# Optimization experiments

Hardware: AMD Instinct MI355X
Metric: run time of the kernel (lower is better)

Reference implementation:

```python
import jax, jax.numpy as jnp
import numpy as np

B, L, D_IN = 8, 512, 1024
HEAD_SIZE = 64
NUM_LABELS = 16
INF = 1e12


def _rotary_sin_cos(seq_len, dim):
    # HF RoFormerSinusoidalPositionalEmbedding: inv_freq = 10000^(-2i/dim)
    pos = np.arange(seq_len, dtype=np.float64)[:, None]
    inv_freq = 1.0 / np.power(10000.0, 2.0 * np.arange(dim // 2) / dim)
    ang = pos * inv_freq  # [L, dim//2]
    # interleave: [s0, s0, s1, s1, ...] (matches stack([sin,sin],-1).reshape)
    sin = jnp.asarray(np.repeat(np.sin(ang), 2, axis=-1), dtype=jnp.float32)
    cos = jnp.asarray(np.repeat(np.cos(ang), 2, axis=-1), dtype=jnp.float32)
    return sin[None], cos[None]  # [1, L, dim]


def _rotate_half(x):
    # [-x1, x0, -x3, x2, ...]
    return jnp.stack([-x[..., 1::2], x[..., ::2]], axis=-1).reshape(x.shape)


def setup_inputs() -> dict:
    key = jax.random.key(0)
    k1, k2, k3, k4, k5 = jax.random.split(key, 5)
    s1 = 1.0 / np.sqrt(D_IN)
    s2 = 1.0 / np.sqrt(2 * HEAD_SIZE)
    return {
        "inputs": jax.random.normal(k1, (B, L, D_IN), dtype=jnp.float32),
        "attention_mask": jnp.ones((B, L), dtype=jnp.int32),
        "W1": jax.random.uniform(k2, (D_IN, 2 * HEAD_SIZE), jnp.float32, -s1, s1),
        "b1": jax.random.uniform(k3, (2 * HEAD_SIZE,), jnp.float32, -s1, s1),
        "W2": jax.random.uniform(k4, (2 * HEAD_SIZE, 2 * NUM_LABELS), jnp.float32, -s2, s2),
        "b2": jax.random.uniform(k5, (2 * NUM_LABELS,), jnp.float32, -s2, s2),
    }


def reference(inputs, attention_mask, W1, b1, W2, b2):
    h = inputs @ W1 + b1                      # [B, L, 2*head_size]
    qw, kw = h[..., ::2], h[..., 1::2]        # [B, L, head_size]

    sin, cos = _rotary_sin_cos(h.shape[1], HEAD_SIZE)
    qw = qw * cos + _rotate_half(qw) * sin
    kw = kw * cos + _rotate_half(kw) * sin

    logits = jnp.einsum("bmd,bnd->bmn", qw, kw) / (HEAD_SIZE ** 0.5)  # [B, L, L]

    bias = (h @ W2 + b2).transpose(0, 2, 1) / 2.0        # [B, 2*heads, L]
    logits = logits[:, None] + bias[:, ::2, None, :] + bias[:, 1::2, :, None]  # [B, heads, L, L]

    am = attention_mask.astype(logits.dtype)
    attn_mask = 1.0 - am[:, None, None, :] * am[:, None, :, None]
    logits = logits - attn_mask * INF

    tril = jnp.tril(jnp.ones((h.shape[1], h.shape[1]), logits.dtype), k=-1)
    logits = logits - tril * INF
    return logits
```

## Files before the change

### kernel.cpp

```cpp
#include <hip/hip_runtime.h>
#include <math.h>

#define B_   8
#define L_   512
#define DIN  1024
#define H_   128
#define HEAD 64
#define NL   16
#define INF_ 1.0e12f

#define SIN_OFF  0
#define COS_OFF  (512*32)
#define QROT_OFF (COS_OFF + 512*32)
#define KROT_OFF (QROT_OFF + B_*L_*HEAD)
#define BQ_OFF   (KROT_OFF + B_*L_*HEAD)
#define BK_OFF   (BQ_OFF + B_*NL*L_)
#define W1T_OFF  (BK_OFF + B_*NL*L_)
#define W2T_OFF  (W1T_OFF + 65536)

typedef float          floatx4  __attribute__((ext_vector_type(4)));
typedef short          shortx8  __attribute__((ext_vector_type(8)));
typedef unsigned short ushortx8 __attribute__((ext_vector_type(8)));

__device__ __forceinline__ unsigned short f2bf(float f) {
    unsigned u = __float_as_uint(f);
    u += 0x7FFFu + ((u >> 16) & 1u);
    return (unsigned short)(u >> 16);
}

__global__ __launch_bounds__(256) void prep_kernel(const float* __restrict__ W1,
                                                   const float* __restrict__ W2,
                                                   float* __restrict__ ws) {
    __shared__ float lds[64 * 132];
    const int tid = threadIdx.x;
    const int bid = blockIdx.x;

    if (bid < 64) {
        int idx = bid * 256 + tid;
        int m = idx >> 5, i = idx & 31;
        double ang = (double)m * pow(10000.0, -(double)i / 32.0);
        ws[SIN_OFF + idx] = (float)sin(ang);
        ws[COS_OFF + idx] = (float)cos(ang);
    } else if (bid < 80) {
        const int k0 = (bid - 64) * 64;
        for (int i = 0; i < 8; i++) {
            int f = tid + i * 256;
            int k = f >> 5, n4 = (f & 31) * 4;
            *(float4*)&lds[k * 132 + n4] = *(const float4*)&W1[(size_t)(k0 + k) * H_ + n4];
        }
        __syncthreads();
        unsigned short* W1T = (unsigned short*)(ws + W1T_OFF);
        const int n  = tid >> 1;
        const int kh = (tid & 1) * 32;
        for (int i = 0; i < 4; i++) {
            ushortx8 p;
            #pragma unroll
            for (int j = 0; j < 8; j++) p[j] = f2bf(lds[(kh + i * 8 + j) * 132 + n]);
            *(ushortx8*)&W1T[(size_t)n * DIN + k0 + kh + i * 8] = p;
        }
    } else {
        unsigned short* W2T = (unsigned short*)(ws + W2T_OFF);
        const int o  = tid >> 3;
        const int kc = (tid & 7) * 16;
        ushortx8 p0, p1;
        #pragma unroll
        for (int j = 0; j < 8; j++) p0[j] = f2bf(W2[(size_t)(kc + j) * 32 + o]);
        #pragma unroll
        for (int j = 0; j < 8; j++) p1[j] = f2bf(W2[(size_t)(kc + 8 + j) * 32 + o]);
        *(ushortx8*)&W2T[(size_t)o * H_ + kc]     = p0;
        *(ushortx8*)&W2T[(size_t)o * H_ + kc + 8] = p1;
    }
}

__global__ __launch_bounds__(256) void gemm1_fused_kernel(
    const float* __restrict__ X, const float* __restrict__ b1,
    const float* __restrict__ b2, float* __restrict__ ws)
{
    __shared__ float hs[16 * 132];

    const int tid  = threadIdx.x;
    const int m0   = blockIdx.x * 16;
    const int w    = tid >> 6;
    const int lane = tid & 63;
    const int lrow = lane >> 4;
    const int lcol = lane & 15;

    const unsigned short* W1T = (const unsigned short*)(ws + W1T_OFF);

    const float* pA = X + (size_t)(m0 + lcol) * DIN + lrow * 8;
    const unsigned short* pB0 = W1T + (size_t)(w * 32 + lcol) * DIN + lrow * 8;
    const unsigned short* pB1 = pB0 + (size_t)16 * DIN;

    floatx4 acc0 = {0.f, 0.f, 0.f, 0.f};
    floatx4 acc1 = {0.f, 0.f, 0.f, 0.f};

    #pragma unroll
    for (int s = 0; s < 32; s++) {
        float4 a0 = *(const float4*)(pA + s * 32);
        float4 a1 = *(const float4*)(pA + s * 32 + 4);
        shortx8 bf0 = *(const shortx8*)(pB0 + s * 32);
        shortx8 bf1 = *(const shortx8*)(pB1 + s * 32);
        ushortx8 afu;
        afu[0] = f2bf(a0.x); afu[1] = f2bf(a0.y); afu[2] = f2bf(a0.z); afu[3] = f2bf(a0.w);
        afu[4] = f2bf(a1.x); afu[5] = f2bf(a1.y); afu[6] = f2bf(a1.z); afu[7] = f2bf(a1.w);
        shortx8 af = (shortx8)afu;
        acc0 = __builtin_amdgcn_mfma_f32_16x16x32_bf16(af, bf0, acc0, 0, 0, 0);
        acc1 = __builtin_amdgcn_mfma_f32_16x16x32_bf16(af, bf1, acc1, 0, 0, 0);
    }

    {
        float b1a = b1[w * 32 + lcol];
        float b1b = b1[w * 32 + 16 + lcol];
        #pragma unroll
        for (int r = 0; r < 4; r++) {
            hs[(lrow * 4 + r) * 132 + w * 32 + lcol]      = acc0[r] + b1a;
            hs[(lrow * 4 + r) * 132 + w * 32 + 16 + lcol] = acc1[r] + b1b;
        }
    }
    __syncthreads();

    {
        int row = tid >> 4;
        int j   = tid & 15;
        int g   = m0 + row;
        int pos = g & (L_ - 1);
        const float* hr = &hs[row * 132];
        float h0 = hr[8 * j + 0], h1 = hr[8 * j + 1];
        float h2 = hr[8 * j + 2], h3 = hr[8 * j + 3];
        float h4 = hr[8 * j + 4], h5 = hr[8 * j + 5];
        float h6 = hr[8 * j + 6], h7 = hr[8 * j + 7];
        float s0 = ws[SIN_OFF + pos * 32 + 2 * j];
        float c0 = ws[COS_OFF + pos * 32 + 2 * j];
        float s1 = ws[SIN_OFF + pos * 32 + 2 * j + 1];
        float c1 = ws[COS_OFF + pos * 32 + 2 * j + 1];
        float4 q, k;
        q.x = h0 * c0 - h2 * s0;  q.y = h2 * c0 + h0 * s0;
        q.z = h4 * c1 - h6 * s1;  q.w = h6 * c1 + h4 * s1;
        k.x = h1 * c0 - h3 * s0;  k.y = h3 * c0 + h1 * s0;
        k.z = h5 * c1 - h7 * s1;  k.w = h7 * c1 + h5 * s1;
        *(float4*)&ws[QROT_OFF + (size_t)g * HEAD + 4 * j] = q;
        *(float4*)&ws[KROT_OFF + (size_t)g * HEAD + 4 * j] = k;
    }

    if (w == 0) {
        const unsigned short* W2T = (const unsigned short*)(ws + W2T_OFF);
        floatx4 bacc0 = {0.f, 0.f, 0.f, 0.f};
        floatx4 bacc1 = {0.f, 0.f, 0.f, 0.f};
        #pragma unroll
        for (int s = 0; s < 4; s++) {
            int k = s * 32 + lrow * 8;
            ushortx8 hfu;
            #pragma unroll
            for (int j = 0; j < 8; j++) hfu[j] = f2bf(hs[lcol * 132 + k + j]);
            shortx8 hf = (shortx8)hfu;
            shortx8 wf0 = *(const shortx8*)(W2T + (size_t)lcol * H_ + k);
            shortx8 wf1 = *(const shortx8*)(W2T + (size_t)(16 + lcol) * H_ + k);
            bacc0 = __builtin_amdgcn_mfma_f32_16x16x32_bf16(hf, wf0, bacc0, 0, 0, 0);
            bacc1 = __builtin_amdgcn_mfma_f32_16x16x32_bf16(hf, wf1, bacc1, 0, 0, 0);
        }
        float b2a = b2[lcol], b2b = b2[16 + lcol];
        #pragma unroll
        for (int r = 0; r < 4; r++) {
            int g   = m0 + lrow * 4 + r;
            int bb  = g >> 9;
            int pos = g & (L_ - 1);
            float v0 = (bacc0[r] + b2a) * 0.5f;
            float v1 = (bacc1[r] + b2b) * 0.5f;
            int o0 = lcol, o1 = 16 + lcol;
            if (o0 & 1) ws[BQ_OFF + ((size_t)bb * NL + (o0 >> 1)) * L_ + pos] = v0;
            else        ws[BK_OFF + ((size_t)bb * NL + (o0 >> 1)) * L_ + pos] = v0;
            if (o1 & 1) ws[BQ_OFF + ((size_t)bb * NL + (o1 >> 1)) * L_ + pos] = v1;
            else        ws[BK_OFF + ((size_t)bb * NL + (o1 >> 1)) * L_ + pos] = v1;
        }
    }
}

__global__ __launch_bounds__(256) void qk_bcast_kernel(
    const int* __restrict__ am, const float* __restrict__ ws, float* __restrict__ out)
{
    __shared__ float Qs[64][68];
    __shared__ float Ks[64][68];
    __shared__ float BQs[16][64];
    __shared__ float BKs[16][64];
    __shared__ float maskM[64];
    __shared__ float maskN[64];

    const int tid = threadIdx.x;
    const int bid = blockIdx.x;
    const int bb = bid >> 6;
    const int mt = (bid >> 3) & 7;
    const int nt = bid & 7;
    const int m0 = mt * 64, n0 = nt * 64;

    {
        int r0   = tid >> 4;
        int dcol = (tid & 15) * 4;
        #pragma unroll
        for (int rr = 0; rr < 4; rr++) {
            int r = r0 + rr * 16;
            float4 q = *(const float4*)&ws[QROT_OFF + ((size_t)(bb * L_ + m0 + r)) * HEAD + dcol];
            float4 k = *(const float4*)&ws[KROT_OFF + ((size_t)(bb * L_ + n0 + r)) * HEAD + dcol];
            Qs[dcol + 0][r] = q.x; Qs[dcol + 1][r] = q.y;
            Qs[dcol + 2][r] = q.z; Qs[dcol + 3][r] = q.w;
            Ks[dcol + 0][r] = k.x; Ks[dcol + 1][r] = k.y;
            Ks[dcol + 2][r] = k.z; Ks[dcol + 3][r] = k.w;
        }
    }
    {
        int l = tid >> 4;
        int c = (tid & 15) * 4;
        *(float4*)&BQs[l][c] = *(const float4*)&ws[BQ_OFF + ((size_t)bb * NL + l) * L_ + m0 + c];
        *(float4*)&BKs[l][c] = *(const float4*)&ws[BK_OFF + ((size_t)bb * NL + l) * L_ + n0 + c];
    }
    if (tid < 64)       maskM[tid]      = (float)am[bb * L_ + m0 + tid];
    else if (tid < 128) maskN[tid - 64] = (float)am[bb * L_ + n0 + (tid - 64)];
    __syncthreads();

    const int ty = tid >> 4;
    const int tx = tid & 15;
    float acc[4][4] = {};
    #pragma unroll 8
    for (int d = 0; d < HEAD; d++) {
        float4 a  = *(const float4*)&Qs[d][ty * 4];
        float4 bv = *(const float4*)&Ks[d][tx * 4];
        acc[0][0] += a.x * bv.x; acc[0][1] += a.x * bv.y; acc[0][2] += a.x * bv.z; acc[0][3] += a.x * bv.w;
        acc[1][0] += a.y * bv.x; acc[1][1] += a.y * bv.y; acc[1][2] += a.y * bv.z; acc[1][3] += a.y * bv.w;
        acc[2][0] += a.z * bv.x; acc[2][1] += a.z * bv.y; acc[2][2] += a.z * bv.z; acc[2][3] += a.z * bv.w;
        acc[3][0] += a.w * bv.x; acc[3][1] += a.w * bv.y; acc[3][2] += a.w * bv.z; acc[3][3] += a.w * bv.w;
    }

    float4 base[4];
    #pragma unroll
    for (int r = 0; r < 4; r++) {
        int m = m0 + ty * 4 + r;
        float mm = maskM[ty * 4 + r];
        #pragma unroll
        for (int c = 0; c < 4; c++) {
            int n = n0 + tx * 4 + c;
            float v = acc[r][c] * 0.125f
                    - (1.0f - mm * maskN[tx * 4 + c]) * INF_
                    - ((n < m) ? INF_ : 0.0f);
            ((float*)&base[r])[c] = v;
        }
    }

    #pragma unroll
    for (int l = 0; l < NL; l++) {
        float4 bk4 = *(const float4*)&BKs[l][tx * 4];
        size_t outb = (((size_t)(bb * NL + l)) * L_ + m0 + ty * 4) * L_ + n0 + tx * 4;
        #pragma unroll
        for (int r = 0; r < 4; r++) {
            float bq = BQs[l][ty * 4 + r];
            float4 o;
            o.x = base[r].x + bk4.x + bq;
            o.y = base[r].y + bk4.y + bq;
            o.z = base[r].z + bk4.z + bq;
            o.w = base[r].w + bk4.w + bq;
            *(float4*)&out[outb + (size_t)r * L_] = o;
        }
    }
}

extern "C" void kernel_launch(void* const* d_in, const int* in_sizes, int n_in,
                              void* d_out, int out_size, void* d_ws, size_t ws_size,
                              hipStream_t stream) {
    const float* X  = (const float*)d_in[0];
    const int*   am = (const int*)d_in[1];
    const float* W1 = (const float*)d_in[2];
    const float* b1 = (const float*)d_in[3];
    const float* W2 = (const float*)d_in[4];
    const float* b2 = (const float*)d_in[5];
    float* out = (float*)d_out;
    float* ws  = (float*)d_ws;

    prep_kernel<<<81, 256, 0, stream>>>(W1, W2, ws);
    gemm1_fused_kernel<<<(B_ * L_) / 16, 256, 0, stream>>>(X, b1, b2, ws);
    qk_bcast_kernel<<<B_ * (L_ / 64) * (L_ / 64), 256, 0, stream>>>(am, ws, out);
}
```

Before: 53.91 us.

## Split GEMM1 K dimension across 16 waves with LDS reduction; float rotary tables

The projection GEMM now runs with 1024-thread blocks. The K=1024 reduction is split four ways across wave groups, and the partial MFMA accumulators are summed in shared memory before the bias and rotary epilogue. This raises memory-level parallelism per row tile, at the cost of a 32KB LDS reduction buffer and an extra barrier. Separately, the sin/cos table generation switches from double-precision pow/sin/cos to single-precision expf/sinf/cosf to cut prep cost, with a small risk to accuracy at large angles.

```diff
diff --git a/kernel.cpp b/kernel.cpp
--- a/kernel.cpp
+++ b/kernel.cpp
@@ -38,9 +38,10 @@
     if (bid < 64) {
         int idx = bid * 256 + tid;
         int m = idx >> 5, i = idx & 31;
-        double ang = (double)m * pow(10000.0, -(double)i / 32.0);
-        ws[SIN_OFF + idx] = (float)sin(ang);
-        ws[COS_OFF + idx] = (float)cos(ang);
+        float freq = expf(-(float)i * 0.28782313662425575f);
+        float ang  = (float)m * freq;
+        ws[SIN_OFF + idx] = sinf(ang);
+        ws[COS_OFF + idx] = cosf(ang);
     } else if (bid < 80) {
         const int k0 = (bid - 64) * 64;
         for (int i = 0; i < 8; i++) {
@@ -72,34 +73,37 @@
     }
 }
 
-__global__ __launch_bounds__(256) void gemm1_fused_kernel(
+__global__ __launch_bounds__(1024, 4) void gemm1_fused_kernel(
     const float* __restrict__ X, const float* __restrict__ b1,
     const float* __restrict__ b2, float* __restrict__ ws)
 {
+    __shared__ float red[8][16][64];
     __shared__ float hs[16 * 132];
 
     const int tid  = threadIdx.x;
     const int m0   = blockIdx.x * 16;
     const int w    = tid >> 6;
+    const int g    = w & 3;
+    const int s    = w >> 2;
     const int lane = tid & 63;
     const int lrow = lane >> 4;
     const int lcol = lane & 15;
 
     const unsigned short* W1T = (const unsigned short*)(ws + W1T_OFF);
 
-    const float* pA = X + (size_t)(m0 + lcol) * DIN + lrow * 8;
-    const unsigned short* pB0 = W1T + (size_t)(w * 32 + lcol) * DIN + lrow * 8;
+    const float* pA = X + (size_t)(m0 + lcol) * DIN + s * 256 + lrow * 8;
+    const unsigned short* pB0 = W1T + (size_t)(g * 32 + lcol) * DIN + s * 256 + lrow * 8;
     const unsigned short* pB1 = pB0 + (size_t)16 * DIN;
 
     floatx4 acc0 = {0.f, 0.f, 0.f, 0.f};
     floatx4 acc1 = {0.f, 0.f, 0.f, 0.f};
 
     #pragma unroll
-    for (int s = 0; s < 32; s++) {
-        float4 a0 = *(const float4*)(pA + s * 32);
-        float4 a1 = *(const float4*)(pA + s * 32 + 4);
-        shortx8 bf0 = *(const shortx8*)(pB0 + s * 32);
-        shortx8 bf1 = *(const shortx8*)(pB1 + s * 32);
+    for (int st = 0; st < 8; st++) {
+        float4 a0 = *(const float4*)(pA + st * 32);
+        float4 a1 = *(const float4*)(pA + st * 32 + 4);
+        shortx8 bf0 = *(const shortx8*)(pB0 + st * 32);
+        shortx8 bf1 = *(const shortx8*)(pB1 + st * 32);
         ushortx8 afu;
         afu[0] = f2bf(a0.x); afu[1] = f2bf(a0.y); afu[2] = f2bf(a0.z); afu[3] = f2bf(a0.w);
         afu[4] = f2bf(a1.x); afu[5] = f2bf(a1.y); afu[6] = f2bf(a1.z); afu[7] = f2bf(a1.w);
@@ -108,22 +112,33 @@
         acc1 = __builtin_amdgcn_mfma_f32_16x16x32_bf16(af, bf1, acc1, 0, 0, 0);
     }
 
-    {
-        float b1a = b1[w * 32 + lcol];
-        float b1b = b1[w * 32 + 16 + lcol];
+    #pragma unroll
+    for (int r = 0; r < 4; r++) {
+        red[r][w][lane]     = acc0[r];
+        red[4 + r][w][lane] = acc1[r];
+    }
+    __syncthreads();
+
+    if (w < 4) {
+        float b1a = b1[g * 32 + lcol];
+        float b1b = b1[g * 32 + 16 + lcol];
         #pragma unroll
         for (int r = 0; r < 4; r++) {
-            hs[(lrow * 4 + r) * 132 + w * 32 + lcol]      = acc0[r] + b1a;
-            hs[(lrow * 4 + r) * 132 + w * 32 + 16 + lcol] = acc1[r] + b1b;
+            float v0 = red[r][g][lane]     + red[r][g + 4][lane]
+                     + red[r][g + 8][lane] + red[r][g + 12][lane];
+            float v1 = red[4 + r][g][lane]     + red[4 + r][g + 4][lane]
+                     + red[4 + r][g + 8][lane] + red[4 + r][g + 12][lane];
+            hs[(lrow * 4 + r) * 132 + g * 32 + lcol]      = v0 + b1a;
+            hs[(lrow * 4 + r) * 132 + g * 32 + 16 + lcol] = v1 + b1b;
         }
     }
     __syncthreads();
 
-    {
+    if (tid < 256) {
         int row = tid >> 4;
         int j   = tid & 15;
-        int g   = m0 + row;
-        int pos = g & (L_ - 1);
+        int gg  = m0 + row;
+        int pos = gg & (L_ - 1);
         const float* hr = &hs[row * 132];
         float h0 = hr[8 * j + 0], h1 = hr[8 * j + 1];
         float h2 = hr[8 * j + 2], h3 = hr[8 * j + 3];
@@ -138,8 +153,8 @@
         q.z = h4 * c1 - h6 * s1;  q.w = h6 * c1 + h4 * s1;
         k.x = h1 * c0 - h3 * s0;  k.y = h3 * c0 + h1 * s0;
         k.z = h5 * c1 - h7 * s1;  k.w = h7 * c1 + h5 * s1;
-        *(float4*)&ws[QROT_OFF + (size_t)g * HEAD + 4 * j] = q;
-        *(float4*)&ws[KROT_OFF + (size_t)g * HEAD + 4 * j] = k;
+        *(float4*)&ws[QROT_OFF + (size_t)gg * HEAD + 4 * j] = q;
+        *(float4*)&ws[KROT_OFF + (size_t)gg * HEAD + 4 * j] = k;
     }
 
     if (w == 0) {
@@ -147,8 +162,8 @@
         floatx4 bacc0 = {0.f, 0.f, 0.f, 0.f};
         floatx4 bacc1 = {0.f, 0.f, 0.f, 0.f};
         #pragma unroll
-        for (int s = 0; s < 4; s++) {
-            int k = s * 32 + lrow * 8;
+        for (int st = 0; st < 4; st++) {
+            int k = st * 32 + lrow * 8;
             ushortx8 hfu;
             #pragma unroll
             for (int j = 0; j < 8; j++) hfu[j] = f2bf(hs[lcol * 132 + k + j]);
@@ -161,9 +176,9 @@
         float b2a = b2[lcol], b2b = b2[16 + lcol];
         #pragma unroll
         for (int r = 0; r < 4; r++) {
-            int g   = m0 + lrow * 4 + r;
-            int bb  = g >> 9;
-            int pos = g & (L_ - 1);
+            int gg  = m0 + lrow * 4 + r;
+            int bb  = gg >> 9;
+            int pos = gg & (L_ - 1);
             float v0 = (bacc0[r] + b2a) * 0.5f;
             float v1 = (bacc1[r] + b2b) * 0.5f;
             int o0 = lcol, o1 = 16 + lcol;
@@ -274,6 +289,6 @@
     float* ws  = (float*)d_ws;
 
     prep_kernel<<<81, 256, 0, stream>>>(W1, W2, ws);
-    gemm1_fused_kernel<<<(B_ * L_) / 16, 256, 0, stream>>>(X, b1, b2, ws);
+    gemm1_fused_kernel<<<(B_ * L_) / 16, 1024, 0, stream>>>(X, b1, b2, ws);
     qk_bcast_kernel<<<B_ * (L_ / 64) * (L_ / 64), 256, 0, stream>>>(am, ws, out);
 }
```

New measurement: 54.01 us. Within noise of the previous version (+0.2%).
